# Optimization experiments

Measured on AMD Instinct MI355X. Metric: run time of the kernel, lower is better.

Reference implementation:

```python
import jax, jax.numpy as jnp
import numpy as np

N_EMBED = 1024
N_HEAD = 16
HEAD_SIZE = N_EMBED // N_HEAD  # 64
SEQ = 2048
BATCH = 2
EPS = 1e-5


def setup_inputs() -> dict:
    key = jax.random.key(0)
    ks = jax.random.split(key, 16)
    s = lambda fan_in: 1.0 / np.sqrt(fan_in)
    d, h, hs, f = N_EMBED, N_HEAD, HEAD_SIZE, 4 * N_EMBED
    return {
        "x": jax.random.normal(ks[0], (BATCH, SEQ, d), dtype=jnp.float32),
        # per-head QKV projections (no bias), stacked over heads: [H, D, hs]
        "wq": jax.random.normal(ks[1], (h, d, hs), dtype=jnp.float32) * s(d),
        "wk": jax.random.normal(ks[2], (h, d, hs), dtype=jnp.float32) * s(d),
        "wv": jax.random.normal(ks[3], (h, d, hs), dtype=jnp.float32) * s(d),
        "w_proj": jax.random.normal(ks[4], (d, d), dtype=jnp.float32) * s(d),
        "b_proj": jnp.zeros((d,), dtype=jnp.float32),
        "w1": jax.random.normal(ks[5], (d, f), dtype=jnp.float32) * s(d),
        "b1": jnp.zeros((f,), dtype=jnp.float32),
        "w2": jax.random.normal(ks[6], (f, d), dtype=jnp.float32) * s(f),
        "b2": jnp.zeros((d,), dtype=jnp.float32),
        "g1": jnp.ones((d,), dtype=jnp.float32),
        "be1": jnp.zeros((d,), dtype=jnp.float32),
        "g2": jnp.ones((d,), dtype=jnp.float32),
        "be2": jnp.zeros((d,), dtype=jnp.float32),
    }


def _layer_norm(x, gamma, beta):
    mu = jnp.mean(x, axis=-1, keepdims=True)
    var = jnp.mean(jnp.square(x - mu), axis=-1, keepdims=True)
    return (x - mu) * jax.lax.rsqrt(var + EPS) * gamma + beta


def reference(x, wq, wk, wv, w_proj, b_proj, w1, b1, w2, b2, g1, be1, g2, be2):
    B, S, D = x.shape
    # per-head projections (vectorized over heads): [B, H, S, hs]
    q = jnp.einsum("bsd,hdk->bhsk", x, wq)
    k = jnp.einsum("bsd,hdk->bhsk", x, wk)
    v = jnp.einsum("bsd,hdk->bhsk", x, wv)
    scale = HEAD_SIZE ** -0.5
    scores = jnp.einsum("bhsk,bhtk->bhst", q, k) * scale  # [B,H,S,S]
    causal = jnp.tril(jnp.ones((S, S), dtype=bool))
    scores = jnp.where(causal, scores, -jnp.inf)
    w = jax.nn.softmax(scores, axis=-1)  # dropout=0 -> identity
    attn = jnp.einsum("bhst,bhtk->bhsk", w, v)  # [B,H,S,hs]
    # concat heads (head-major ordering matches torch.cat over heads)
    attn = attn.transpose(0, 2, 1, 3).reshape(B, S, D)
    y = attn @ w_proj + b_proj
    x = _layer_norm(x + y, g1, be1)
    y = jax.nn.relu(x @ w1 + b1) @ w2 + b2
    x = _layer_norm(x + y, g2, be2)
    return x
```

## Files before the change

kernel.cpp:

```cpp
#include <hip/hip_runtime.h>


typedef unsigned short u16;
typedef unsigned int u32;
typedef __attribute__((ext_vector_type(8))) short bf16x8;
typedef __attribute__((ext_vector_type(4))) float f32x4;
typedef __attribute__((ext_vector_type(2))) u32 u32x2;
typedef __attribute__((ext_vector_type(4))) _Float16 f16x4;

#define MFMA16(a, b, c) __builtin_amdgcn_mfma_f32_16x16x32_bf16(a, b, c, 0, 0, 0)
#define MFMAH(a, b, c) __builtin_amdgcn_mfma_f32_16x16x16f16(a, b, c, 0, 0, 0)

__device__ __forceinline__ u16 f2b(float f) {
  unsigned int u = __builtin_bit_cast(unsigned int, f);
  u = (u + 0x7fffu + ((u >> 16) & 1u)) >> 16;
  return (u16)u;
}

__device__ __forceinline__ void gload_lds16(const u16* g, u16* l) {
  __builtin_amdgcn_global_load_lds((const __attribute__((address_space(1))) void*)g,
                                   (__attribute__((address_space(3))) void*)l, 16, 0, 0);
}

__device__ __forceinline__ u32 pkrtz(float lo, float hi) {
  return __builtin_bit_cast(u32, __builtin_amdgcn_cvt_pkrtz(lo, hi));
}

__device__ __forceinline__ f16x4 pack4h(float a, float b, float c, float d) {
  u32x2 r = {pkrtz(a, b), pkrtz(c, d)};
  return __builtin_bit_cast(f16x4, r);
}

__device__ __forceinline__ u16 f2h(float v) {
  return __builtin_bit_cast(u16, (_Float16)v);
}


__global__ __launch_bounds__(256) void pack_all(
    const float* __restrict__ x, const float* __restrict__ wq,
    const float* __restrict__ wk, const float* __restrict__ wv,
    const float* __restrict__ wp, const float* __restrict__ w1,
    const float* __restrict__ w2, u16* __restrict__ Xbf, u16* __restrict__ WqkvT,
    u16* __restrict__ WprojT, u16* __restrict__ W1T, u16* __restrict__ W2T) {
  int bid = blockIdx.x;
  int t = threadIdx.x;
  if (bid >= 12288) {
    size_t i = ((size_t)(bid - 12288) * 256 + t) * 4;
    float4 v = *(const float4*)(x + i);
    Xbf[i + 0] = f2b(v.x);
    Xbf[i + 1] = f2b(v.y);
    Xbf[i + 2] = f2b(v.z);
    Xbf[i + 3] = f2b(v.w);
    return;
  }
  __shared__ float tile[32][33];
  int tx = t & 31, ty = t >> 5;
  const float* src;
  u16* dst;
  int R, C, r0, c0;
  float scale = 1.0f;
  if (bid < 3072) {
    int z = bid >> 6, q = bid & 63;
    int p = z >> 4, h = z & 15;
    src = (p == 0 ? wq : (p == 1 ? wk : wv)) + (size_t)h * 1024 * 64;
    scale = (p == 0) ? 0.1803368801f : 1.0f;
    dst = WqkvT + (size_t)(p * 1024 + h * 64) * 1024;
    R = 1024; C = 64;
    c0 = (q & 1) * 32; r0 = (q >> 1) * 32;
  } else if (bid < 4096) {
    int q = bid - 3072;
    src = wp; dst = WprojT; R = 1024; C = 1024;
    c0 = (q & 31) * 32; r0 = (q >> 5) * 32;
  } else if (bid < 8192) {
    int q = bid - 4096;
    src = w1; dst = W1T; R = 1024; C = 4096;
    c0 = (q & 127) * 32; r0 = (q >> 7) * 32;
  } else {
    int q = bid - 8192;
    src = w2; dst = W2T; R = 4096; C = 1024;
    c0 = (q & 31) * 32; r0 = (q >> 5) * 32;
  }
#pragma unroll
  for (int i = 0; i < 4; ++i)
    tile[ty + i * 8][tx] = src[(size_t)(r0 + ty + i * 8) * C + c0 + tx];
  __syncthreads();
#pragma unroll
  for (int i = 0; i < 4; ++i)
    dst[(size_t)(c0 + ty + i * 8) * R + r0 + tx] = f2b(tile[tx][ty + i * 8] * scale);
}


template <int MODE>
__global__ __launch_bounds__(256, 4) void gemm_bf16(const u16* __restrict__ A,
                                                    const u16* __restrict__ Bt, int M,
                                                    int N, int Kc, int lda,
                                                    const float* __restrict__ bias,
                                                    u16* __restrict__ outB, int ldc,
                                                    u16* __restrict__ vtg) {
  constexpr int BM = 128, BN = 128, BK = 64;
  constexpr int IM = 4, JN = 4;
  __shared__ u16 As[BM * BK];
  __shared__ u16 Bs[BN * BK];
  int t = threadIdx.x;
  int m0 = blockIdx.x * BM, n0 = blockIdx.y * BN;
  int kb = blockIdx.z * Kc;
  int lane = t & 63, wid = t >> 6;
  int wm = (wid >> 1) * 64, wn = (wid & 1) * 64;
  int m16 = lane & 15, quad = lane >> 4;
  int sw = m16 & 7;

  f32x4 acc[IM][JN] = {};

  for (int k0 = kb; k0 < kb + Kc; k0 += BK) {
    __syncthreads();
#pragma unroll
    for (int i = 0; i < 4; ++i) {
      int S = i * 256 + t;
      int row = S >> 3, c = S & 7;
      gload_lds16(&A[(size_t)(m0 + row) * lda + k0 + (c ^ (row & 7)) * 8],
                  &As[(i * 256 + wid * 64) * 8]);
    }
#pragma unroll
    for (int i = 0; i < 4; ++i) {
      int S = i * 256 + t;
      int row = S >> 3, c = S & 7;
      gload_lds16(&Bt[(size_t)(n0 + row) * lda + k0 + (c ^ (row & 7)) * 8],
                  &Bs[(i * 256 + wid * 64) * 8]);
    }
    __syncthreads();
#pragma unroll
    for (int kk = 0; kk < 2; ++kk) {
      bf16x8 af[IM], bfr[JN];
      int slot = (kk * 4 + quad) ^ sw;
#pragma unroll
      for (int i = 0; i < IM; ++i)
        af[i] = *(const bf16x8*)&As[(wm + i * 16 + m16) * BK + slot * 8];
#pragma unroll
      for (int j = 0; j < JN; ++j)
        bfr[j] = *(const bf16x8*)&Bs[(wn + j * 16 + m16) * BK + slot * 8];
#pragma unroll
      for (int i = 0; i < IM; ++i)
#pragma unroll
        for (int j = 0; j < JN; ++j) acc[i][j] = MFMA16(af[i], bfr[j], acc[i][j]);
    }
  }

  if (MODE == 3 && n0 >= 2048) {
#pragma unroll
    for (int i = 0; i < IM; ++i)
#pragma unroll
      for (int j = 0; j < JN; ++j) {
        int dg = n0 + wn + j * 16 + m16 - 2048;
        int hh = dg >> 6, dd = dg & 63;
        int token = m0 + wm + i * 16 + quad * 4;
        int bb = token >> 11, tt = token & 2047;
        u32x2 pv = {pkrtz(acc[i][j][0], acc[i][j][1]),
                    pkrtz(acc[i][j][2], acc[i][j][3])};
        *(u32x2*)&vtg[(((size_t)bb * 16 + hh) * 64 + dd) * 2048 + tt] = pv;
      }
    return;
  }

  u16* pb = (MODE == 4) ? outB + (size_t)blockIdx.z * M * N : outB;
#pragma unroll
  for (int i = 0; i < IM; ++i)
#pragma unroll
    for (int j = 0; j < JN; ++j) {
      int col = n0 + wn + j * 16 + m16;
      float bv = (MODE == 1) ? bias[col] : 0.0f;
#pragma unroll
      for (int r = 0; r < 4; ++r) {
        int row = m0 + wm + i * 16 + quad * 4 + r;
        float v = acc[i][j][r];
        if (MODE == 1) {
          v += bv;
          v = v > 0.0f ? v : 0.0f;
          pb[(size_t)row * ldc + col] = f2b(v);
        } else if (MODE == 4) {
          pb[(size_t)row * ldc + col] = f2h(v);
        } else {
          pb[(size_t)row * ldc + col] = f2b(v);
        }
      }
    }
}


__constant__ unsigned char R_QB[32] = {7, 6, 11, 11, 5, 10, 10, 9, 9, 4, 8,
                                       8, 3, 15, 15, 15, 15, 14, 14, 14, 13, 13,
                                       13, 13, 12, 12, 12, 2, 14, 12, 1, 0};
__constant__ unsigned char R_K0[32] = {0, 0, 0, 12, 0, 0, 11, 0, 10, 0, 0,
                                       9, 0, 0, 8, 16, 24, 0, 8, 16, 0, 7,
                                       14, 21, 0, 7, 14, 0, 24, 21, 0, 0};
__constant__ unsigned char R_NIT[32] = {16, 14, 12, 12, 12, 11, 11, 10, 10, 10, 9,
                                        9, 8, 8, 8, 8, 8, 8, 8, 8, 7, 7,
                                        7, 7, 7, 7, 7, 6, 6, 5, 4, 2};
__constant__ unsigned char R_ST[32] = {255, 255, 6, 7, 255, 4, 5, 2, 3, 255, 0,
                                       1, 255, 20, 21, 22, 23, 16, 17, 18, 12, 13,
                                       14, 15, 8, 9, 10, 255, 19, 11, 255, 255};
__constant__ unsigned char CB_BASE[8] = {0, 2, 4, 6, 8, 12, 16, 20};

__global__ __launch_bounds__(256) void attn_part(const u16* __restrict__ qk,
                                                 const u16* __restrict__ vtg,
                                                 u16* __restrict__ attn_out,
                                                 u16* __restrict__ opart,
                                                 float2* __restrict__ ml) {
  int rank = blockIdx.x >> 5, bh = blockIdx.x & 31;
  int qb = R_QB[rank];
  int k_start = R_K0[rank] * 64;
  int iters = R_NIT[rank];
  int st = R_ST[rank];
  int b = bh >> 4, h = bh & 15;

  int t = threadIdx.x, lane = t & 63, w = t >> 6;
  int m16 = lane & 15, quad = lane >> 4;
  int wq0 = qb * 128 + w * 32;

  __shared__ u16 Ks[2][64 * 64];
  __shared__ u16 Vs[2][64 * 64];

  bf16x8 qa[2][2];
#pragma unroll
  for (int qs = 0; qs < 2; ++qs) {
    const u16* qp = qk + (size_t)(b * 2048 + wq0 + qs * 16 + m16) * 2048 + h * 64;
    qa[qs][0] = *(const bf16x8*)&qp[quad * 8];
    qa[qs][1] = *(const bf16x8*)&qp[32 + quad * 8];
  }

  f32x4 oT[2][4] = {};
  f32x4 lacc[2] = {};
  float mrun[2] = {-1e30f, -1e30f};

  int row0 = t >> 3, c0 = t & 7;
  int row1 = 32 + row0;
  const u16* kbase = qk + (size_t)(b * 2048) * 2048 + 1024 + h * 64;
  const u16* vbase = vtg + ((size_t)(b * 16 + h) * 64) * 2048;
  int sw = m16 & 7;

#define STAGE_ASYNC(T0, BUF)                                                        \
  {                                                                                 \
    gload_lds16(&kbase[(size_t)((T0) + row0) * 2048 + (c0 ^ (row0 & 7)) * 8],       \
                &Ks[BUF][(w * 64) * 8]);                                            \
    gload_lds16(&kbase[(size_t)((T0) + row1) * 2048 + (c0 ^ (row1 & 7)) * 8],       \
                &Ks[BUF][(256 + w * 64) * 8]);                                      \
    gload_lds16(&vbase[(size_t)row0 * 2048 + (T0) + (c0 ^ (row0 & 7)) * 8],         \
                &Vs[BUF][(w * 64) * 8]);                                            \
    gload_lds16(&vbase[(size_t)row1 * 2048 + (T0) + (c0 ^ (row1 & 7)) * 8],         \
                &Vs[BUF][(256 + w * 64) * 8]);                                      \
  }

  STAGE_ASYNC(k_start, 0);
  __syncthreads();

  for (int it = 0; it < iters; ++it) {
    int t0 = k_start + it * 64;
    int cur = it & 1;
    if (it + 1 < iters) STAGE_ASYNC(t0 + 64, !cur);

    if (t0 <= wq0 + 31) {
      f32x4 sv[2][4];
#pragma unroll
      for (int ts = 0; ts < 4; ++ts) {
        bf16x8 ka0 = *(const bf16x8*)&Ks[cur][(ts * 16 + m16) * 64 + (quad ^ sw) * 8];
        bf16x8 ka1 =
            *(const bf16x8*)&Ks[cur][(ts * 16 + m16) * 64 + ((4 + quad) ^ sw) * 8];
#pragma unroll
        for (int qs = 0; qs < 2; ++qs) {
          f32x4 a = {};
          a = MFMA16(ka0, qa[qs][0], a);
          a = MFMA16(ka1, qa[qs][1], a);
          sv[qs][ts] = a;
        }
      }
      if (t0 + 63 > wq0) {
#pragma unroll
        for (int qs = 0; qs < 2; ++qs)
#pragma unroll
          for (int ts = 0; ts < 4; ++ts)
#pragma unroll
            for (int rr = 0; rr < 4; ++rr) {
              int key = t0 + ts * 16 + quad * 4 + rr;
              if (key > wq0 + qs * 16 + m16) sv[qs][ts][rr] = -3e38f;
            }
      }
#pragma unroll
      for (int qs = 0; qs < 2; ++qs) {
        float mx = fmaxf(fmaxf(sv[qs][0][0], sv[qs][0][1]),
                         fmaxf(sv[qs][0][2], sv[qs][0][3]));
#pragma unroll
        for (int ts = 1; ts < 4; ++ts)
          mx = fmaxf(mx, fmaxf(fmaxf(sv[qs][ts][0], sv[qs][ts][1]),
                               fmaxf(sv[qs][ts][2], sv[qs][ts][3])));
        mx = fmaxf(mx, __shfl_xor(mx, 16));
        mx = fmaxf(mx, __shfl_xor(mx, 32));
        float mnew = fmaxf(mrun[qs], mx);
        float alpha = exp2f(mrun[qs] - mnew);
        mrun[qs] = mnew;
        lacc[qs] *= alpha;
#pragma unroll
        for (int ds = 0; ds < 4; ++ds) oT[qs][ds] *= alpha;
      }
      f16x4 pf[2][4];
#pragma unroll
      for (int qs = 0; qs < 2; ++qs)
#pragma unroll
        for (int ts = 0; ts < 4; ++ts) {
          float p0 = exp2f(sv[qs][ts][0] - mrun[qs]);
          float p1 = exp2f(sv[qs][ts][1] - mrun[qs]);
          float p2 = exp2f(sv[qs][ts][2] - mrun[qs]);
          float p3 = exp2f(sv[qs][ts][3] - mrun[qs]);
          lacc[qs][0] += p0;
          lacc[qs][1] += p1;
          lacc[qs][2] += p2;
          lacc[qs][3] += p3;
          pf[qs][ts] = pack4h(p0, p1, p2, p3);
        }
#pragma unroll
      for (int ts = 0; ts < 4; ++ts)
#pragma unroll
        for (int ds = 0; ds < 4; ++ds) {
          f16x4 av = __builtin_bit_cast(
              f16x4, *(const u32x2*)&Vs[cur][(ds * 16 + m16) * 64 +
                                             (((ts * 2 + (quad >> 1)) ^ sw) * 8) +
                                             (quad & 1) * 4]);
          oT[0][ds] = MFMAH(av, pf[0][ts], oT[0][ds]);
          oT[1][ds] = MFMAH(av, pf[1][ts], oT[1][ds]);
        }
    }
    __syncthreads();
  }
#undef STAGE_ASYNC

  if (st == 255) {
#pragma unroll
    for (int qs = 0; qs < 2; ++qs) {
      float ls = lacc[qs][0] + lacc[qs][1] + lacc[qs][2] + lacc[qs][3];
      ls += __shfl_xor(ls, 16);
      ls += __shfl_xor(ls, 32);
      float rl = 1.0f / ls;
      int q = wq0 + qs * 16 + m16;
#pragma unroll
      for (int ds = 0; ds < 4; ++ds) {
        f32x4 o = oT[qs][ds];
        u32x2 ov = {(u32)f2b(o[0] * rl) | ((u32)f2b(o[1] * rl) << 16),
                    (u32)f2b(o[2] * rl) | ((u32)f2b(o[3] * rl) << 16)};
        *(u32x2*)&attn_out[(size_t)(b * 2048 + q) * 1024 + h * 64 + ds * 16 +
                           quad * 4] = ov;
      }
    }
  } else {
    size_t sbase = ((size_t)st * 32 + bh) * 128;
#pragma unroll
    for (int qs = 0; qs < 2; ++qs) {
      float ls = lacc[qs][0] + lacc[qs][1] + lacc[qs][2] + lacc[qs][3];
      ls += __shfl_xor(ls, 16);
      ls += __shfl_xor(ls, 32);
      int qloc = w * 32 + qs * 16 + m16;
#pragma unroll
      for (int ds = 0; ds < 4; ++ds) {
        f32x4 o = oT[qs][ds];
        u32x2 ov = {pkrtz(o[0], o[1]), pkrtz(o[2], o[3])};
        *(u32x2*)&opart[(sbase + qloc) * 64 + ds * 16 + quad * 4] = ov;
      }
      if (quad == 0) ml[sbase + qloc] = make_float2(mrun[qs], ls);
    }
  }
}

__global__ __launch_bounds__(256) void attn_comb(const u16* __restrict__ opart,
                                                 const float2* __restrict__ ml,
                                                 u16* __restrict__ attn_out) {
  int qb = 8 + blockIdx.x, bh = blockIdx.y;
  int b = bh >> 4, h = bh & 15;
  int nseg = (qb < 12) ? 2 : 4;
  int base = CB_BASE[qb - 8];
  int t = threadIdx.x;
  int q = t >> 1, dh = (t & 1) * 32;

  float m[4], l[4], wgt[4];
  float M = -3e38f;
  for (int s = 0; s < nseg; ++s) {
    float2 v = ml[((size_t)(base + s) * 32 + bh) * 128 + q];
    m[s] = v.x;
    l[s] = v.y;
    M = fmaxf(M, v.x);
  }
  float lsum = 0.0f;
  for (int s = 0; s < nseg; ++s) {
    wgt[s] = exp2f(m[s] - M);
    lsum += wgt[s] * l[s];
  }
  float rl = 1.0f / lsum;

  size_t orow = (size_t)(b * 2048 + qb * 128 + q) * 1024 + h * 64 + dh;
#pragma unroll 2
  for (int dd = 0; dd < 32; dd += 4) {
    float o0 = 0, o1 = 0, o2 = 0, o3 = 0;
    for (int s = 0; s < nseg; ++s) {
      f16x4 hv = __builtin_bit_cast(
          f16x4, *(const u32x2*)&opart[(((size_t)(base + s) * 32 + bh) * 128 + q) * 64 +
                                       dh + dd]);
      o0 += wgt[s] * (float)hv[0];
      o1 += wgt[s] * (float)hv[1];
      o2 += wgt[s] * (float)hv[2];
      o3 += wgt[s] * (float)hv[3];
    }
    u32x2 ov = {(u32)f2b(o0 * rl) | ((u32)f2b(o1 * rl) << 16),
                (u32)f2b(o2 * rl) | ((u32)f2b(o3 * rl) << 16)};
    *(u32x2*)&attn_out[orow + dd] = ov;
  }
}


__global__ __launch_bounds__(256) void ln_comb(const u16* __restrict__ parts, int np,
                                               const float* __restrict__ bias,
                                               const float* __restrict__ resid,
                                               const float* __restrict__ g,
                                               const float* __restrict__ be,
                                               float* __restrict__ outF,
                                               u16* __restrict__ outB) {
  int row = blockIdx.x;
  int t = threadIdx.x;
  size_t off = (size_t)row * 1024 + t * 4;
  float4 bv4 = *(const float4*)(bias + t * 4);
  float a0 = bv4.x, a1 = bv4.y, a2 = bv4.z, a3 = bv4.w;
  for (int c = 0; c < np; ++c) {
    f16x4 hv =
        __builtin_bit_cast(f16x4, *(const u32x2*)&parts[(size_t)c * 4096 * 1024 + off]);
    a0 += (float)hv[0];
    a1 += (float)hv[1];
    a2 += (float)hv[2];
    a3 += (float)hv[3];
  }
  float4 rv = *(const float4*)(resid + off);
  a0 += rv.x;
  a1 += rv.y;
  a2 += rv.z;
  a3 += rv.w;

  float s = a0 + a1 + a2 + a3;
  float sq = a0 * a0 + a1 * a1 + a2 * a2 + a3 * a3;
#pragma unroll
  for (int d = 1; d < 64; d <<= 1) {
    s += __shfl_xor(s, d);
    sq += __shfl_xor(sq, d);
  }
  __shared__ float red[8];
  int lane = t & 63, wid = t >> 6;
  if (lane == 0) {
    red[wid] = s;
    red[4 + wid] = sq;
  }
  __syncthreads();
  s = red[0] + red[1] + red[2] + red[3];
  sq = red[4] + red[5] + red[6] + red[7];
  float mu = s * (1.0f / 1024.0f);
  float var = sq * (1.0f / 1024.0f) - mu * mu;
  float rstd = rsqrtf(var + 1e-5f);
  float4 gv = *(const float4*)(g + t * 4);
  float4 bev = *(const float4*)(be + t * 4);
  float o0 = (a0 - mu) * rstd * gv.x + bev.x;
  float o1 = (a1 - mu) * rstd * gv.y + bev.y;
  float o2 = (a2 - mu) * rstd * gv.z + bev.z;
  float o3 = (a3 - mu) * rstd * gv.w + bev.w;
  if (outF) {
    float4 ov = {o0, o1, o2, o3};
    *(float4*)(outF + off) = ov;
  }
  if (outB) {
    outB[off + 0] = f2b(o0);
    outB[off + 1] = f2b(o1);
    outB[off + 2] = f2b(o2);
    outB[off + 3] = f2b(o3);
  }
}


extern "C" void kernel_launch(void* const* d_in, const int* in_sizes, int n_in,
                              void* d_out, int out_size, void* d_ws, size_t ws_size,
                              hipStream_t stream) {
  const float* x = (const float*)d_in[0];
  const float* wq = (const float*)d_in[1];
  const float* wk = (const float*)d_in[2];
  const float* wv = (const float*)d_in[3];
  const float* w_proj = (const float*)d_in[4];
  const float* b_proj = (const float*)d_in[5];
  const float* w1 = (const float*)d_in[6];
  const float* b1 = (const float*)d_in[7];
  const float* w2 = (const float*)d_in[8];
  const float* b2 = (const float*)d_in[9];
  const float* g1 = (const float*)d_in[10];
  const float* be1 = (const float*)d_in[11];
  const float* g2 = (const float*)d_in[12];
  const float* be2 = (const float*)d_in[13];
  float* out = (float*)d_out;

  const int M = 4096;
  char* w = (char*)d_ws;
  u16* Xbf = (u16*)w;        w += (size_t)M * 1024 * 2;
  u16* WqkvT = (u16*)w;      w += (size_t)3072 * 1024 * 2;
  u16* WprojT = (u16*)w;     w += (size_t)1024 * 1024 * 2;
  u16* W1T = (u16*)w;        w += (size_t)4096 * 1024 * 2;
  u16* X1b = (u16*)w;        w += (size_t)M * 1024 * 2;
  u16* W2T = (u16*)w;        w += (size_t)1024 * 4096 * 2;
  u16* QK = (u16*)w;         w += (size_t)M * 2048 * 2;
  u16* Vtg = (u16*)w;        w += (size_t)2 * 16 * 64 * 2048 * 2;
  u16* Attn = (u16*)w;       w += (size_t)M * 1024 * 2;
  float* X1f = (float*)w;    w += (size_t)M * 1024 * 4;

  u16* Pdown = Xbf;
  u16* Pproj = QK;
  u16* Hbuf = QK;
  u16* Opart = (u16*)X1f;
  float2* Ml = (float2*)((char*)X1f + (size_t)13 * 1024 * 1024);

  pack_all<<<16384, 256, 0, stream>>>(x, wq, wk, wv, w_proj, w1, w2, Xbf, WqkvT,
                                      WprojT, W1T, W2T);

  gemm_bf16<3><<<dim3(32, 24, 1), 256, 0, stream>>>(Xbf, WqkvT, M, 3072, 1024, 1024,
                                                    nullptr, QK, 2048, Vtg);

  attn_part<<<1024, 256, 0, stream>>>(QK, Vtg, Attn, Opart, Ml);
  attn_comb<<<dim3(8, 32), 256, 0, stream>>>(Opart, Ml, Attn);

  gemm_bf16<4><<<dim3(32, 8, 2), 256, 0, stream>>>(Attn, WprojT, M, 1024, 512, 1024,
                                                   nullptr, Pproj, 1024, nullptr);
  ln_comb<<<M, 256, 0, stream>>>(Pproj, 2, b_proj, x, g1, be1, X1f, X1b);

  gemm_bf16<1><<<dim3(32, 32, 1), 256, 0, stream>>>(X1b, W1T, M, 4096, 1024, 1024, b1,
                                                    Hbuf, 4096, nullptr);

  gemm_bf16<4><<<dim3(32, 8, 4), 256, 0, stream>>>(Hbuf, W2T, M, 1024, 1024, 4096,
                                                   nullptr, Pdown, 1024, nullptr);
  ln_comb<<<M, 256, 0, stream>>>(Pdown, 4, b2, X1f, g2, be2, out, nullptr);
}
```

Before: 327.4 us.

## Use 32x32 MFMA in GEMM and MFMA-based softmax row sums in attention

The GEMM inner loop moves from 16x16x32 to 32x32x16 bf16 MFMA tiles, so each wave issues fewer matrix instructions and fewer LDS fragment loads per K step. In attention, the per-lane softmax denominator adds and the shuffle reductions are replaced by an extra f16 MFMA that multiplies the P tile by a ones vector. The online-softmax rescale is also skipped with a wave-uniform ballot when no row max grew. In exchange, the row sums are accumulated from f16-rounded probabilities, and the 32x32 tile layout changes the epilogue store pattern.

```diff
diff --git a/kernel.cpp b/kernel.cpp
--- a/kernel.cpp
+++ b/kernel.cpp
@@ -5,9 +5,11 @@
 typedef unsigned int u32;
 typedef __attribute__((ext_vector_type(8))) short bf16x8;
 typedef __attribute__((ext_vector_type(4))) float f32x4;
+typedef __attribute__((ext_vector_type(16))) float f32x16;
 typedef __attribute__((ext_vector_type(2))) u32 u32x2;
 typedef __attribute__((ext_vector_type(4))) _Float16 f16x4;
 
+#define MFMA32(a, b, c) __builtin_amdgcn_mfma_f32_32x32x16_bf16(a, b, c, 0, 0, 0)
 #define MFMA16(a, b, c) __builtin_amdgcn_mfma_f32_16x16x32_bf16(a, b, c, 0, 0, 0)
 #define MFMAH(a, b, c) __builtin_amdgcn_mfma_f32_16x16x16f16(a, b, c, 0, 0, 0)
 
@@ -98,7 +100,6 @@
                                                     u16* __restrict__ outB, int ldc,
                                                     u16* __restrict__ vtg) {
   constexpr int BM = 128, BN = 128, BK = 64;
-  constexpr int IM = 4, JN = 4;
   __shared__ u16 As[BM * BK];
   __shared__ u16 Bs[BN * BK];
   int t = threadIdx.x;
@@ -106,10 +107,10 @@
   int kb = blockIdx.z * Kc;
   int lane = t & 63, wid = t >> 6;
   int wm = (wid >> 1) * 64, wn = (wid & 1) * 64;
-  int m16 = lane & 15, quad = lane >> 4;
-  int sw = m16 & 7;
-
-  f32x4 acc[IM][JN] = {};
+  int m32 = lane & 31, half = lane >> 5;
+  int sw = m32 & 7;
+
+  f32x16 acc[2][2] = {};
 
   for (int k0 = kb; k0 < kb + Kc; k0 += BK) {
     __syncthreads();
@@ -129,57 +130,63 @@
     }
     __syncthreads();
 #pragma unroll
-    for (int kk = 0; kk < 2; ++kk) {
-      bf16x8 af[IM], bfr[JN];
-      int slot = (kk * 4 + quad) ^ sw;
-#pragma unroll
-      for (int i = 0; i < IM; ++i)
-        af[i] = *(const bf16x8*)&As[(wm + i * 16 + m16) * BK + slot * 8];
-#pragma unroll
-      for (int j = 0; j < JN; ++j)
-        bfr[j] = *(const bf16x8*)&Bs[(wn + j * 16 + m16) * BK + slot * 8];
-#pragma unroll
-      for (int i = 0; i < IM; ++i)
-#pragma unroll
-        for (int j = 0; j < JN; ++j) acc[i][j] = MFMA16(af[i], bfr[j], acc[i][j]);
+    for (int ks = 0; ks < 4; ++ks) {
+      int slot = (ks * 2 + half) ^ sw;
+      bf16x8 af[2], bfr[2];
+#pragma unroll
+      for (int i = 0; i < 2; ++i)
+        af[i] = *(const bf16x8*)&As[(wm + i * 32 + m32) * BK + slot * 8];
+#pragma unroll
+      for (int j = 0; j < 2; ++j)
+        bfr[j] = *(const bf16x8*)&Bs[(wn + j * 32 + m32) * BK + slot * 8];
+#pragma unroll
+      for (int i = 0; i < 2; ++i)
+#pragma unroll
+        for (int j = 0; j < 2; ++j) acc[i][j] = MFMA32(af[i], bfr[j], acc[i][j]);
     }
   }
 
   if (MODE == 3 && n0 >= 2048) {
 #pragma unroll
-    for (int i = 0; i < IM; ++i)
-#pragma unroll
-      for (int j = 0; j < JN; ++j) {
-        int dg = n0 + wn + j * 16 + m16 - 2048;
+    for (int i = 0; i < 2; ++i)
+#pragma unroll
+      for (int j = 0; j < 2; ++j) {
+        int dg = n0 + wn + j * 32 + m32 - 2048;
         int hh = dg >> 6, dd = dg & 63;
-        int token = m0 + wm + i * 16 + quad * 4;
-        int bb = token >> 11, tt = token & 2047;
-        u32x2 pv = {pkrtz(acc[i][j][0], acc[i][j][1]),
-                    pkrtz(acc[i][j][2], acc[i][j][3])};
-        *(u32x2*)&vtg[(((size_t)bb * 16 + hh) * 64 + dd) * 2048 + tt] = pv;
+#pragma unroll
+        for (int g = 0; g < 4; ++g) {
+          int token = m0 + wm + i * 32 + g * 8 + half * 4;
+          int bb = token >> 11, tt = token & 2047;
+          u32x2 pv = {pkrtz(acc[i][j][g * 4 + 0], acc[i][j][g * 4 + 1]),
+                      pkrtz(acc[i][j][g * 4 + 2], acc[i][j][g * 4 + 3])};
+          *(u32x2*)&vtg[(((size_t)bb * 16 + hh) * 64 + dd) * 2048 + tt] = pv;
+        }
       }
     return;
   }
 
   u16* pb = (MODE == 4) ? outB + (size_t)blockIdx.z * M * N : outB;
 #pragma unroll
-  for (int i = 0; i < IM; ++i)
-#pragma unroll
-    for (int j = 0; j < JN; ++j) {
-      int col = n0 + wn + j * 16 + m16;
+  for (int i = 0; i < 2; ++i)
+#pragma unroll
+    for (int j = 0; j < 2; ++j) {
+      int col = n0 + wn + j * 32 + m32;
       float bv = (MODE == 1) ? bias[col] : 0.0f;
 #pragma unroll
-      for (int r = 0; r < 4; ++r) {
-        int row = m0 + wm + i * 16 + quad * 4 + r;
-        float v = acc[i][j][r];
-        if (MODE == 1) {
-          v += bv;
-          v = v > 0.0f ? v : 0.0f;
-          pb[(size_t)row * ldc + col] = f2b(v);
-        } else if (MODE == 4) {
-          pb[(size_t)row * ldc + col] = f2h(v);
-        } else {
-          pb[(size_t)row * ldc + col] = f2b(v);
+      for (int g = 0; g < 4; ++g) {
+        int row = m0 + wm + i * 32 + g * 8 + half * 4;
+#pragma unroll
+        for (int rr = 0; rr < 4; ++rr) {
+          float v = acc[i][j][g * 4 + rr];
+          if (MODE == 1) {
+            v += bv;
+            v = v > 0.0f ? v : 0.0f;
+            pb[(size_t)(row + rr) * ldc + col] = f2b(v);
+          } else if (MODE == 4) {
+            pb[(size_t)(row + rr) * ldc + col] = f2h(v);
+          } else {
+            pb[(size_t)(row + rr) * ldc + col] = f2b(v);
+          }
         }
       }
     }
@@ -228,8 +235,12 @@
   }
 
   f32x4 oT[2][4] = {};
-  f32x4 lacc[2] = {};
+  f32x4 oL[2] = {};
   float mrun[2] = {-1e30f, -1e30f};
+
+  f16x4 ones;
+#pragma unroll
+  for (int j = 0; j < 4; ++j) ones[j] = (_Float16)1.0f;
 
   int row0 = t >> 3, c0 = t & 7;
   int row1 = 32 + row0;
@@ -283,6 +294,7 @@
               if (key > wq0 + qs * 16 + m16) sv[qs][ts][rr] = -3e38f;
             }
       }
+      f16x4 pf[2][4];
 #pragma unroll
       for (int qs = 0; qs < 2; ++qs) {
         float mx = fmaxf(fmaxf(sv[qs][0][0], sv[qs][0][1]),
@@ -293,28 +305,24 @@
                                fmaxf(sv[qs][ts][2], sv[qs][ts][3])));
         mx = fmaxf(mx, __shfl_xor(mx, 16));
         mx = fmaxf(mx, __shfl_xor(mx, 32));
-        float mnew = fmaxf(mrun[qs], mx);
-        float alpha = exp2f(mrun[qs] - mnew);
-        mrun[qs] = mnew;
-        lacc[qs] *= alpha;
-#pragma unroll
-        for (int ds = 0; ds < 4; ++ds) oT[qs][ds] *= alpha;
-      }
-      f16x4 pf[2][4];
-#pragma unroll
-      for (int qs = 0; qs < 2; ++qs)
+        if (__ballot(mx > mrun[qs])) {
+          float mnew = fmaxf(mrun[qs], mx);
+          float alpha = exp2f(mrun[qs] - mnew);
+          mrun[qs] = mnew;
+          oL[qs] *= alpha;
+#pragma unroll
+          for (int ds = 0; ds < 4; ++ds) oT[qs][ds] *= alpha;
+        }
 #pragma unroll
         for (int ts = 0; ts < 4; ++ts) {
           float p0 = exp2f(sv[qs][ts][0] - mrun[qs]);
           float p1 = exp2f(sv[qs][ts][1] - mrun[qs]);
           float p2 = exp2f(sv[qs][ts][2] - mrun[qs]);
           float p3 = exp2f(sv[qs][ts][3] - mrun[qs]);
-          lacc[qs][0] += p0;
-          lacc[qs][1] += p1;
-          lacc[qs][2] += p2;
-          lacc[qs][3] += p3;
           pf[qs][ts] = pack4h(p0, p1, p2, p3);
+          oL[qs] = MFMAH(ones, pf[qs][ts], oL[qs]);
         }
+      }
 #pragma unroll
       for (int ts = 0; ts < 4; ++ts)
 #pragma unroll
@@ -334,10 +342,7 @@
   if (st == 255) {
 #pragma unroll
     for (int qs = 0; qs < 2; ++qs) {
-      float ls = lacc[qs][0] + lacc[qs][1] + lacc[qs][2] + lacc[qs][3];
-      ls += __shfl_xor(ls, 16);
-      ls += __shfl_xor(ls, 32);
-      float rl = 1.0f / ls;
+      float rl = 1.0f / oL[qs][0];
       int q = wq0 + qs * 16 + m16;
 #pragma unroll
       for (int ds = 0; ds < 4; ++ds) {
@@ -352,9 +357,6 @@
     size_t sbase = ((size_t)st * 32 + bh) * 128;
 #pragma unroll
     for (int qs = 0; qs < 2; ++qs) {
-      float ls = lacc[qs][0] + lacc[qs][1] + lacc[qs][2] + lacc[qs][3];
-      ls += __shfl_xor(ls, 16);
-      ls += __shfl_xor(ls, 32);
       int qloc = w * 32 + qs * 16 + m16;
 #pragma unroll
       for (int ds = 0; ds < 4; ++ds) {
@@ -362,7 +364,7 @@
         u32x2 ov = {pkrtz(o[0], o[1]), pkrtz(o[2], o[3])};
         *(u32x2*)&opart[(sbase + qloc) * 64 + ds * 16 + quad * 4] = ov;
       }
-      if (quad == 0) ml[sbase + qloc] = make_float2(mrun[qs], ls);
+      if (quad == 0) ml[sbase + qloc] = make_float2(mrun[qs], oL[qs][0]);
     }
   }
 }
```

After: 348.2 us. 6.3% more time.
